# Kernel optimization log

Hardware: AMD Instinct MI355X
Metric: run time of the kernel (lower is better)

The kernel has to match this reference:

```python
import jax, jax.numpy as jnp
import numpy as np

B, T, C, H, K = 4, 2048, 2048, 32, 64
CHUNK = 64  # matches `splits = 64` in the torch source
EPS = 0.00064


def setup_inputs() -> dict:
    key = jax.random.key(0)
    ks = jax.random.split(key, 16)
    return {
        "x": jax.random.normal(ks[0], (B, T, C), jnp.float32),
        "state": jax.random.normal(ks[1], (1, 1, C), jnp.float32) * 0.1,
        "wkvstate": jax.random.normal(ks[2], (H, K, K), jnp.float32) * 0.02,
        "time_mix_k": jax.random.uniform(ks[3], (1, 1, C), jnp.float32),
        "time_mix_v": jax.random.uniform(ks[4], (1, 1, C), jnp.float32),
        "time_mix_r": jax.random.uniform(ks[5], (1, 1, C), jnp.float32),
        "time_mix_g": jax.random.uniform(ks[6], (1, 1, C), jnp.float32),
        "time_decay": jax.random.normal(ks[7], (H, K), jnp.float32) * 0.5,
        "time_faaaa": jax.random.normal(ks[8], (H, K), jnp.float32) * 0.1,
        "w_r": jax.random.normal(ks[9], (C, C), jnp.float32) * 0.02,
        "w_k": jax.random.normal(ks[10], (C, C), jnp.float32) * 0.02,
        "w_v": jax.random.normal(ks[11], (C, C), jnp.float32) * 0.02,
        "w_g": jax.random.normal(ks[12], (C, C), jnp.float32) * 0.02,
        "w_o": jax.random.normal(ks[13], (C, C), jnp.float32) * 0.02,
        "ln_w": jnp.ones((C,), jnp.float32),
        "ln_b": jnp.zeros((C,), jnp.float32),
    }


def reference(x, state, wkvstate, time_mix_k, time_mix_v, time_mix_r, time_mix_g,
              time_decay, time_faaaa, w_r, w_k, w_v, w_g, w_o, ln_w, ln_b):
    Bx, Tx, Cx = x.shape
    Hx, Kx = time_decay.shape

    # TimeShift (training path): prepend learned state, drop last token
    xx = jnp.concatenate([jnp.broadcast_to(state, (Bx, 1, Cx)), x[:, :-1]], axis=1)
    xk = x * time_mix_k + xx * (1.0 - time_mix_k)
    xv = x * time_mix_v + xx * (1.0 - time_mix_v)
    xr = x * time_mix_r + xx * (1.0 - time_mix_r)
    xg = x * time_mix_g + xx * (1.0 - time_mix_g)

    g = jax.nn.silu(xg @ w_g.T)  # (B,T,C)

    def to_heads(t):  # (B,T,C) -> (B,H,T,K)
        return t.reshape(Bx, Tx, Hx, Kx).transpose(0, 2, 1, 3)

    r = to_heads(xr @ w_r.T)
    k = to_heads(xk @ w_k.T)
    v = to_heads(xv @ w_v.T)

    w = jnp.exp(-jnp.exp(time_decay))  # (H,K), per-channel decay in (0,1)
    t_idx = jnp.arange(Tx)
    wfor = w[None, :, None, :] ** t_idx[None, None, :, None]          # w^t
    wback = w[None, :, None, :] ** (Tx - 1 - t_idx)[None, None, :, None]  # w^(T-1-t)

    # contribution of the incoming wkv state: (r * w^t) @ S0
    base = jnp.einsum('bhtk,hkj->bhtj', r * wfor, wkvstate)
    # bonus (u) diagonal term: sum_k(k_t * u * r_t) * v_t
    base = base + jnp.sum(k * r * time_faaaa[None, :, None, :], axis=-1, keepdims=True) * v

    kw = k * wback  # k_t scaled by w^(T-1-t), as in the source

    # strict-past causal product on shifted slices (r[:,1:] vs kw/v[:,:-1]),
    # computed chunk-by-chunk exactly like the blocked tril loop.
    rr, kk, vv = r[:, :, 1:], kw[:, :, :-1], v[:, :, :-1]
    Tm = Tx - 1
    pad = (-Tm) % CHUNK
    pd = lambda a: jnp.pad(a, ((0, 0), (0, 0), (0, pad), (0, 0)))
    rr, kk, vv = pd(rr), pd(kk), pd(vv)
    nC = (Tm + pad) // CHUNK
    resh = lambda a: a.reshape(Bx, Hx, nC, CHUNK, Kx).transpose(2, 0, 1, 3, 4)
    rc_, kc_, vc_ = resh(rr), resh(kk), resh(vv)
    mask = jnp.tril(jnp.ones((CHUNK, CHUNK), bool))  # q <= p (inclusive) == tril(i-j) globally

    def step(S, inp):
        rc, kc, vc = inp  # (B,H,CHUNK,K)
        att = jnp.einsum('bhpk,bhqk->bhpq', rc, kc)
        att = jnp.where(mask, att, 0.0)
        out = jnp.einsum('bhpq,bhqk->bhpk', att, vc) + jnp.einsum('bhpk,bhkj->bhpj', rc, S)
        S = S + jnp.einsum('bhqk,bhqj->bhkj', kc, vc)
        return S, out

    S0 = jnp.zeros((Bx, Hx, Kx, Kx), x.dtype)
    _, outs = jax.lax.scan(step, S0, (rc_, kc_, vc_))  # (nC,B,H,CHUNK,K)
    intra = outs.transpose(1, 2, 0, 3, 4).reshape(Bx, Hx, nC * CHUNK, Kx)[:, :, :Tm]
    wkv = base.at[:, :, 1:].add(intra)  # (B,H,T,K)

    # GroupNorm(n_head groups) after a bf16 round-trip, as in the source
    y = wkv.transpose(0, 2, 1, 3)  # (B,T,H,K)
    y = y.astype(jnp.bfloat16).astype(jnp.float32)
    mu = jnp.mean(y, axis=-1, keepdims=True)
    var = jnp.var(y, axis=-1, keepdims=True)
    y = (y - mu) / jnp.sqrt(var + EPS)
    y = y * ln_w.reshape(Hx, Kx) + ln_b.reshape(Hx, Kx)
    y = y.reshape(Bx, Tx, Cx)

    return (y * g) @ w_o.T
```

## Files before the change

### kernel.cpp

```cpp
#include <hip/hip_runtime.h>

#define Bn 4
#define Tn 2048
#define Cn 2048
#define Hn 32
#define Mn 8192
#define EPSV 0.00064f
#define SEGS 16
#define ZTHR 96.f

typedef __attribute__((ext_vector_type(4))) float f32x4;
typedef _Float16 half4 __attribute__((ext_vector_type(4)));
typedef _Float16 half8 __attribute__((ext_vector_type(8)));

#if defined(__has_builtin)
#if __has_builtin(__builtin_amdgcn_fdot2)
#define HAS_FDOT2 1
#endif
#endif
#ifndef HAS_FDOT2
#define HAS_FDOT2 0
#endif

#define SWZ(row, col) ((col) ^ ((((row) >> 2) & 7) << 3))

__device__ __forceinline__ unsigned short f2bf(float f) {
  unsigned int u = __float_as_uint(f);
  u += 0x7fffu + ((u >> 16) & 1u);
  return (unsigned short)(u >> 16);
}
__device__ __forceinline__ float bf2f(unsigned short h) {
  return __uint_as_float(((unsigned int)h) << 16);
}

__device__ __forceinline__ float dot8(half8 a, half8 b, float acc) {
#if HAS_FDOT2
  acc = __builtin_amdgcn_fdot2(__builtin_shufflevector(a, a, 0, 1),
                               __builtin_shufflevector(b, b, 0, 1), acc, false);
  acc = __builtin_amdgcn_fdot2(__builtin_shufflevector(a, a, 2, 3),
                               __builtin_shufflevector(b, b, 2, 3), acc, false);
  acc = __builtin_amdgcn_fdot2(__builtin_shufflevector(a, a, 4, 5),
                               __builtin_shufflevector(b, b, 4, 5), acc, false);
  acc = __builtin_amdgcn_fdot2(__builtin_shufflevector(a, a, 6, 7),
                               __builtin_shufflevector(b, b, 6, 7), acc, false);
#else
#pragma unroll
  for (int i = 0; i < 8; ++i) acc += (float)a[i] * (float)b[i];
#endif
  return acc;
}

__global__ __launch_bounds__(256) void wcast_f16_kernel(
    const float* __restrict__ src, _Float16* __restrict__ dst) {
  const size_t e = ((size_t)blockIdx.x * 256 + threadIdx.x) * 4;
  const float4 v = *(const float4*)(src + e);
  half4 h;
  h.x = (_Float16)v.x; h.y = (_Float16)v.y; h.z = (_Float16)v.z; h.w = (_Float16)v.w;
  *(half4*)(dst + e) = h;
}

__global__ __launch_bounds__(256) void mix4_kernel(
    const float* __restrict__ x, const float* __restrict__ state,
    const float* __restrict__ tmr, const float* __restrict__ tmk,
    const float* __restrict__ tmv, const float* __restrict__ tmg,
    _Float16* __restrict__ xr, _Float16* __restrict__ xk,
    _Float16* __restrict__ xv, _Float16* __restrict__ xg) {
  const size_t e = ((size_t)blockIdx.x * 256 + threadIdx.x) * 4;
  const int c = (int)(e & (Cn - 1));
  const int t = (int)((e >> 11) & (Tn - 1));
  float4 xv_ = *(const float4*)(x + e);
  float4 xx  = (t == 0) ? *(const float4*)(state + c) : *(const float4*)(x + e - Cn);
  float4 dx; dx.x = xv_.x - xx.x; dx.y = xv_.y - xx.y; dx.z = xv_.z - xx.z; dx.w = xv_.w - xx.w;
  const float* tms[4] = {tmr, tmk, tmv, tmg};
  _Float16* dsts[4] = {xr, xk, xv, xg};
#pragma unroll
  for (int s = 0; s < 4; ++s) {
    float4 m = *(const float4*)(tms[s] + c);
    half4 o;
    o.x = (_Float16)(xx.x + dx.x * m.x);
    o.y = (_Float16)(xx.y + dx.y * m.y);
    o.z = (_Float16)(xx.z + dx.z * m.z);
    o.w = (_Float16)(xx.w + dx.w * m.w);
    *(half4*)(dsts[s] + e) = o;
  }
}

template <int OUT_F16>
__global__ __launch_bounds__(512, 2) void gemm256_kernel(
    const _Float16* __restrict__ A, const _Float16* __restrict__ W,
    void* __restrict__ Ov) {
  __shared__ _Float16 As[4][256 * 32];
  __shared__ _Float16 Bs[4][256 * 32];
  const int tid = threadIdx.x;
  const int wid = tid >> 6, ln = tid & 63;
  const int wm = wid >> 2, wn = wid & 3;
  const int m16 = ln & 15, qd = ln >> 4;

  const int bid = blockIdx.x;
  const int mtile = ((bid & 7) << 2) | ((bid >> 3) & 3);
  const int ntile = bid >> 5;

  const _Float16* Ab = A + (size_t)mtile * 256 * Cn;
  const _Float16* Wb = W + (size_t)ntile * 256 * Cn;

  const _Float16* gA[2]; const _Float16* gB[2];
  int lof[2];
#pragma unroll
  for (int i = 0; i < 2; ++i) {
    int r = ((wid * 2 + i) << 4) + (ln >> 2);
    int q = (ln & 3) ^ ((ln >> 2) & 3) ^ ((ln >> 4) & 3);
    gA[i] = Ab + (size_t)r * Cn + (q << 3);
    gB[i] = Wb + (size_t)r * Cn + (q << 3);
    lof[i] = ((wid * 2 + i) << 10);
  }
  const int swz = (qd ^ (m16 & 3) ^ ((m16 >> 2) & 3)) << 4;
  const int aob = (wm * 128 + m16) * 64 + swz;
  const int bob = (wn * 64 + m16) * 64 + swz;

  f32x4 acc[8][4];
#pragma unroll
  for (int i = 0; i < 8; ++i)
#pragma unroll
    for (int j = 0; j < 4; ++j) acc[i][j] = 0.f;

#define STAGE(slot, k0)                                                              \
  {                                                                                  \
    _Pragma("unroll") for (int i_ = 0; i_ < 2; ++i_) {                               \
      __builtin_amdgcn_global_load_lds(                                              \
          (const __attribute__((address_space(1))) void*)(gA[i_] + (k0)),            \
          (__attribute__((address_space(3))) void*)((char*)&As[slot][0] + lof[i_]),  \
          16, 0, 0);                                                                 \
      __builtin_amdgcn_global_load_lds(                                              \
          (const __attribute__((address_space(1))) void*)(gB[i_] + (k0)),            \
          (__attribute__((address_space(3))) void*)((char*)&Bs[slot][0] + lof[i_]),  \
          16, 0, 0);                                                                 \
    }                                                                                \
  }

  STAGE(0, 0);
  STAGE(1, 32);

  const int NT = Cn / 32;
  for (int t = 0; t < NT; ++t) {
    const int sl = t & 3;
    if (t + 2 < NT) {
      STAGE((t + 2) & 3, (t + 2) * 32);
      asm volatile("s_waitcnt vmcnt(8)" ::: "memory");
    } else if (t + 1 < NT) {
      asm volatile("s_waitcnt vmcnt(4)" ::: "memory");
    } else {
      asm volatile("s_waitcnt vmcnt(0)" ::: "memory");
    }
    __builtin_amdgcn_s_barrier();

    const char* Abase = (const char*)&As[sl][0];
    const char* Bbase = (const char*)&Bs[sl][0];
    half8 bfr[4];
#pragma unroll
    for (int nf = 0; nf < 4; ++nf)
      bfr[nf] = *(const half8*)(Bbase + nf * 1024 + bob);
    half8 af[8];
#pragma unroll
    for (int fr = 0; fr < 8; ++fr)
      af[fr] = *(const half8*)(Abase + fr * 1024 + aob);
    __builtin_amdgcn_s_setprio(1);
#pragma unroll
    for (int fr = 0; fr < 8; ++fr)
#pragma unroll
      for (int nf = 0; nf < 4; ++nf)
        acc[fr][nf] = __builtin_amdgcn_mfma_f32_16x16x32_f16(af[fr], bfr[nf], acc[fr][nf], 0, 0, 0);
    __builtin_amdgcn_s_setprio(0);
  }
#undef STAGE

  const size_t obase = (size_t)mtile * 256 * Cn + (size_t)ntile * 256;
#pragma unroll
  for (int fr = 0; fr < 8; ++fr) {
#pragma unroll
    for (int nf = 0; nf < 4; ++nf) {
      int col  = wn * 64 + nf * 16 + m16;
      int row0 = wm * 128 + fr * 16 + (qd << 2);
      f32x4 cv = acc[fr][nf];
      if constexpr (OUT_F16) {
        _Float16* Ob = (_Float16*)Ov + obase;
#pragma unroll
        for (int rg = 0; rg < 4; ++rg)
          Ob[(size_t)(row0 + rg) * Cn + col] = (_Float16)cv[rg];
      } else {
        float* Ob = (float*)Ov + obase;
#pragma unroll
        for (int rg = 0; rg < 4; ++rg)
          Ob[(size_t)(row0 + rg) * Cn + col] = cv[rg];
      }
    }
  }
}

__global__ __launch_bounds__(256) void seg_sum_kernel(
    const _Float16* __restrict__ kA, const _Float16* __restrict__ vA,
    const float* __restrict__ td, _Float16* __restrict__ segsum) {
  __shared__ float sK[32][68];
  __shared__ float sV[32][68];
  __shared__ float sEw[64];
  __shared__ float sEwMin;
  const int tid = threadIdx.x;
  const int bh = blockIdx.x;
  const int seg = SEGS - 1 - blockIdx.y;
  const int b = bh >> 5, h = bh & 31;
  const size_t colbase = (size_t)b * Tn * Cn + h * 64;
  const _Float16* kG = kA + colbase;
  const _Float16* vG = vA + colbase;

  if (tid < 64) sEw[tid] = __expf(td[h * 64 + tid]);
  __syncthreads();
  if (tid == 0) {
    float mn = sEw[0];
    for (int i = 1; i < 64; ++i) mn = fminf(mn, sEw[i]);
    sEwMin = mn;
  }
  __syncthreads();

  const int uk0 = (tid >> 4) << 2;
  const int uj0 = (tid & 15) << 2;
  float su[16];
#pragma unroll
  for (int i = 0; i < 16; ++i) su[i] = 0.f;

  const int c0 = seg * (64 / SEGS), c1 = c0 + (64 / SEGS);
  for (int c = c0; c < c1; ++c) {
    const int tb = c << 5;
    if ((float)(Tn - 32 - tb) * sEwMin >= ZTHR) continue;
#pragma unroll
    for (int rep = 0; rep < 2; ++rep) {
      int f4 = tid + (rep << 8);
      int row = f4 >> 4;
      int col = (f4 & 15) << 2;
      int t = tb + row;
      size_t off = (size_t)t * Cn + col;
      half4 ku = *(const half4*)(kG + off);
      half4 vu = *(const half4*)(vG + off);
      float4 vf; vf.x = (float)vu.x; vf.y = (float)vu.y; vf.z = (float)vu.z; vf.w = (float)vu.w;
      *(float4*)&sV[row][col] = vf;
      float e = (float)(Tn - 1 - t);
      float4 kw;
      kw.x = (float)ku.x * __expf(-e * sEw[col + 0]);
      kw.y = (float)ku.y * __expf(-e * sEw[col + 1]);
      kw.z = (float)ku.z * __expf(-e * sEw[col + 2]);
      kw.w = (float)ku.w * __expf(-e * sEw[col + 3]);
      *(float4*)&sK[row][col] = kw;
    }
    __syncthreads();
    for (int q = 0; q < 32; ++q) {
      float4 kq = *(const float4*)&sK[q][uk0];
      float4 vq = *(const float4*)&sV[q][uj0];
      su[0]  += kq.x * vq.x; su[1]  += kq.x * vq.y; su[2]  += kq.x * vq.z; su[3]  += kq.x * vq.w;
      su[4]  += kq.y * vq.x; su[5]  += kq.y * vq.y; su[6]  += kq.y * vq.z; su[7]  += kq.y * vq.w;
      su[8]  += kq.z * vq.x; su[9]  += kq.z * vq.y; su[10] += kq.z * vq.z; su[11] += kq.z * vq.w;
      su[12] += kq.w * vq.x; su[13] += kq.w * vq.y; su[14] += kq.w * vq.z; su[15] += kq.w * vq.w;
    }
    __syncthreads();
  }
  _Float16* dst = segsum + ((size_t)bh * SEGS + seg) * 4096;
#pragma unroll
  for (int i = 0; i < 4; ++i) {
    half4 s;
    s.x = (_Float16)su[i * 4 + 0]; s.y = (_Float16)su[i * 4 + 1];
    s.z = (_Float16)su[i * 4 + 2]; s.w = (_Float16)su[i * 4 + 3];
    *(half4*)(dst + (uk0 + i) * 64 + uj0) = s;
  }
}

__global__ __launch_bounds__(256) void scan_kernel(
    const _Float16* __restrict__ rA, const _Float16* __restrict__ kA,
    const _Float16* __restrict__ vA, const _Float16* __restrict__ gA,
    const float* __restrict__ wkvst, const float* __restrict__ td,
    const float* __restrict__ faaaa, const float* __restrict__ lnw,
    const float* __restrict__ lnb, const _Float16* __restrict__ segsum,
    _Float16* __restrict__ A2) {
  __shared__ __align__(16) _Float16 sR[32][72];
  __shared__ __align__(16) _Float16 sK[32][72];
  __shared__ __align__(16) _Float16 sV[32][72];
  __shared__ __align__(16) _Float16 sRW[32][72];
  __shared__ __align__(16) _Float16 sS0[64][72];
  __shared__ float sS[64][68];
  __shared__ float sAtt[32][36];
  __shared__ float sEw[64];
  __shared__ float sU[64];
  __shared__ float sDotP[32][8];
  __shared__ float sRedM[32][8];
  __shared__ float sRedQ[32][8];
  __shared__ float sMV[32][2];
  __shared__ float sEwMin;
  const int tid = threadIdx.x;
  const int bh = blockIdx.x;
  const int seg = SEGS - 1 - blockIdx.y;
  const int b = bh >> 5, h = bh & 31;
  const size_t colbase = (size_t)b * Tn * Cn + h * 64;
  const _Float16* rG = rA + colbase;
  const _Float16* kG = kA + colbase;
  const _Float16* vG = vA + colbase;
  const _Float16* gG = gA + colbase;
  _Float16* outG = A2 + colbase;

  if (tid < 64) {
    sEw[tid] = __expf(td[h * 64 + tid]);
    sU[tid]  = faaaa[h * 64 + tid];
  }
  {
    float4 acc4[4];
#pragma unroll
    for (int j = 0; j < 4; ++j) { acc4[j].x = 0.f; acc4[j].y = 0.f; acc4[j].z = 0.f; acc4[j].w = 0.f; }
    for (int sp = 0; sp < seg; ++sp) {
      const _Float16* basep = segsum + ((size_t)bh * SEGS + sp) * 4096;
#pragma unroll
      for (int j = 0; j < 4; ++j) {
        int f4 = tid + j * 256;
        int row = f4 >> 4, c4 = (f4 & 15) << 2;
        half4 m = *(const half4*)(basep + row * 64 + c4);
        acc4[j].x += (float)m.x; acc4[j].y += (float)m.y;
        acc4[j].z += (float)m.z; acc4[j].w += (float)m.w;
      }
    }
#pragma unroll
    for (int j = 0; j < 4; ++j) {
      int f4 = tid + j * 256;
      int row = f4 >> 4, c4 = (f4 & 15) << 2;
      *(float4*)&sS[row][c4] = acc4[j];
    }
    int row = tid >> 2, c0 = (tid & 3) << 4;
    const float* sp = wkvst + (size_t)h * 4096 + row * 64 + c0;
    float4 f0 = *(const float4*)(sp);
    float4 f1 = *(const float4*)(sp + 4);
    float4 f2 = *(const float4*)(sp + 8);
    float4 f3 = *(const float4*)(sp + 12);
    half8 h0, h1;
    h0[0] = (_Float16)f0.x; h0[1] = (_Float16)f0.y; h0[2] = (_Float16)f0.z; h0[3] = (_Float16)f0.w;
    h0[4] = (_Float16)f1.x; h0[5] = (_Float16)f1.y; h0[6] = (_Float16)f1.z; h0[7] = (_Float16)f1.w;
    h1[0] = (_Float16)f2.x; h1[1] = (_Float16)f2.y; h1[2] = (_Float16)f2.z; h1[3] = (_Float16)f2.w;
    h1[4] = (_Float16)f3.x; h1[5] = (_Float16)f3.y; h1[6] = (_Float16)f3.z; h1[7] = (_Float16)f3.w;
    *(half8*)&sS0[row][SWZ(row, c0)] = h0;
    *(half8*)&sS0[row][SWZ(row, c0 + 8)] = h1;
  }
  __syncthreads();
  if (tid == 0) {
    float mn = sEw[0];
    for (int i = 1; i < 64; ++i) mn = fminf(mn, sEw[i]);
    sEwMin = mn;
  }
  __syncthreads();

  const int ap  = tid >> 3;
  const int aq0 = (tid & 7) << 2;
  const int oj0 = (tid & 7) << 3;
  const int uk0 = (tid >> 4) << 2;
  const int uj0 = (tid & 15) << 2;
  const int srow = tid >> 3;
  const int scol = (tid & 7) << 3;
  float lw[8], lb[8];
#pragma unroll
  for (int i = 0; i < 8; ++i) { lw[i] = lnw[h * 64 + oj0 + i]; lb[i] = lnb[h * 64 + oj0 + i]; }

  bool snz = (seg > 0) && ((float)(Tn - seg * (Tn / SEGS)) * sEwMin < ZTHR);

  const int c0 = seg * (64 / SEGS), c1 = c0 + (64 / SEGS);
  for (int c = c0; c < c1; ++c) {
    const int tb = c << 5;
    const bool skipc  = ((float)(Tn - 32 - tb) * sEwMin) >= ZTHR;
    const bool active = ((float)tb * sEwMin) < 88.f;
    {
      int t = tb + srow;
      size_t off = (size_t)t * Cn + scol;
      half8 ru = *(const half8*)(rG + off);
      half8 ku = *(const half8*)(kG + off);
      half8 vu = *(const half8*)(vG + off);
      *(half8*)&sV[srow][SWZ(srow, scol)] = vu;
      float dp = 0.f;
#pragma unroll
      for (int i = 0; i < 8; ++i) dp += (float)ku[i] * (float)ru[i] * sU[scol + i];
      sDotP[srow][tid & 7] = dp;
      if (!skipc) {
        *(half8*)&sR[srow][SWZ(srow, scol)] = ru;
        float e = (float)(Tn - 1 - t);
        half8 kwh;
#pragma unroll
        for (int i = 0; i < 8; ++i)
          kwh[i] = (_Float16)((float)ku[i] * __expf(-e * sEw[scol + i]));
        *(half8*)&sK[srow][SWZ(srow, scol)] = kwh;
      }
      if (active) {
        float tt = (float)t;
        half8 rwh;
#pragma unroll
        for (int i = 0; i < 8; ++i)
          rwh[i] = (_Float16)((float)ru[i] * __expf(-tt * sEw[scol + i]));
        *(half8*)&sRW[srow][SWZ(srow, scol)] = rwh;
      }
    }
    __syncthreads();
    if (!skipc) {
      float a4[4] = {0.f, 0.f, 0.f, 0.f};
      for (int k = 0; k < 64; k += 8) {
        half8 rv = *(const half8*)&sR[ap][SWZ(ap, k)];
#pragma unroll
        for (int qq = 0; qq < 4; ++qq) {
          int row = aq0 + qq;
          half8 kv = *(const half8*)&sK[row][SWZ(row, k)];
          a4[qq] = dot8(rv, kv, a4[qq]);
        }
      }
#pragma unroll
      for (int qq = 0; qq < 4; ++qq)
        sAtt[ap][aq0 + qq] = ((aq0 + qq) < ap) ? a4[qq] : 0.f;
      __syncthreads();
    }
    float y[8];
    {
      float o[8];
#pragma unroll
      for (int i = 0; i < 8; ++i) o[i] = 0.f;
      if (!skipc) {
        for (int q = 0; q < 32; ++q) {
          float aw = sAtt[ap][q];
          half8 vv = *(const half8*)&sV[q][SWZ(q, oj0)];
#pragma unroll
          for (int i = 0; i < 8; ++i) o[i] += aw * (float)vv[i];
        }
      }
      if (snz) {
        for (int k8 = 0; k8 < 64; k8 += 8) {
          half8 rv = *(const half8*)&sR[ap][SWZ(ap, k8)];
#pragma unroll
          for (int kk = 0; kk < 8; ++kk) {
            float rw = (float)rv[kk];
            const float* srow_ = &sS[k8 + kk][oj0];
            float4 s0 = *(const float4*)(srow_);
            float4 s1 = *(const float4*)(srow_ + 4);
            o[0] += rw * s0.x; o[1] += rw * s0.y; o[2] += rw * s0.z; o[3] += rw * s0.w;
            o[4] += rw * s1.x; o[5] += rw * s1.y; o[6] += rw * s1.z; o[7] += rw * s1.w;
          }
        }
      }
      if (active) {
        for (int k8 = 0; k8 < 64; k8 += 8) {
          half8 rv = *(const half8*)&sRW[ap][SWZ(ap, k8)];
#pragma unroll
          for (int kk = 0; kk < 8; ++kk) {
            float rw = (float)rv[kk];
            int k = k8 + kk;
            half8 s08 = *(const half8*)&sS0[k][SWZ(k, oj0)];
#pragma unroll
            for (int i = 0; i < 8; ++i) o[i] += rw * (float)s08[i];
          }
        }
      }
      float dot = 0.f;
#pragma unroll
      for (int s = 0; s < 8; ++s) dot += sDotP[ap][s];
      half8 vme = *(const half8*)&sV[ap][SWZ(ap, oj0)];
#pragma unroll
      for (int i = 0; i < 8; ++i) o[i] += dot * (float)vme[i];
      float sm = 0.f, sq = 0.f;
#pragma unroll
      for (int i = 0; i < 8; ++i) {
        y[i] = bf2f(f2bf(o[i]));
        sm += y[i]; sq += y[i] * y[i];
      }
      sRedM[ap][tid & 7] = sm; sRedQ[ap][tid & 7] = sq;
    }
    __syncthreads();
    if ((tid & 7) == 0) {
      float sm = 0.f, sq = 0.f;
#pragma unroll
      for (int i = 0; i < 8; ++i) { sm += sRedM[ap][i]; sq += sRedQ[ap][i]; }
      float mu = sm * (1.f / 64.f);
      float var = sq * (1.f / 64.f) - mu * mu;
      sMV[ap][0] = mu; sMV[ap][1] = rsqrtf(var + EPSV);
    }
    __syncthreads();
    {
      float mu = sMV[ap][0], rs = sMV[ap][1];
      int t = tb + ap;
      size_t off = (size_t)t * Cn + oj0;
      half8 g8 = *(const half8*)(gG + off);
      half8 o8;
#pragma unroll
      for (int i = 0; i < 8; ++i) {
        float gv = (float)g8[i];
        float yn = (y[i] - mu) * rs * lw[i] + lb[i];
        float gs = gv / (1.f + __expf(-gv));
        o8[i] = (_Float16)(yn * gs);
      }
      *(half8*)(outG + off) = o8;
    }
    if (!skipc) {
      float su[16];
#pragma unroll
      for (int i = 0; i < 4; ++i) {
        float4 s = *(const float4*)&sS[uk0 + i][uj0];
        su[i * 4 + 0] = s.x; su[i * 4 + 1] = s.y; su[i * 4 + 2] = s.z; su[i * 4 + 3] = s.w;
      }
      for (int q = 0; q < 32; ++q) {
        half4 kq4 = *(const half4*)&sK[q][SWZ(q, uk0)];
        half4 vq4 = *(const half4*)&sV[q][SWZ(q, uj0)];
        float kx = (float)kq4.x, ky = (float)kq4.y, kz = (float)kq4.z, kw_ = (float)kq4.w;
        float vx = (float)vq4.x, vy = (float)vq4.y, vz = (float)vq4.z, vw = (float)vq4.w;
        su[0]  += kx * vx; su[1]  += kx * vy; su[2]  += kx * vz; su[3]  += kx * vw;
        su[4]  += ky * vx; su[5]  += ky * vy; su[6]  += ky * vz; su[7]  += ky * vw;
        su[8]  += kz * vx; su[9]  += kz * vy; su[10] += kz * vz; su[11] += kz * vw;
        su[12] += kw_ * vx; su[13] += kw_ * vy; su[14] += kw_ * vz; su[15] += kw_ * vw;
      }
#pragma unroll
      for (int i = 0; i < 4; ++i) {
        float4 s; s.x = su[i * 4 + 0]; s.y = su[i * 4 + 1]; s.z = su[i * 4 + 2]; s.w = su[i * 4 + 3];
        *(float4*)&sS[uk0 + i][uj0] = s;
      }
      snz = true;
      __syncthreads();
    }
  }
}

extern "C" void kernel_launch(void* const* d_in, const int* in_sizes, int n_in,
                              void* d_out, int out_size, void* d_ws, size_t ws_size,
                              hipStream_t stream) {
  const float* x     = (const float*)d_in[0];
  const float* state = (const float*)d_in[1];
  const float* wkvst = (const float*)d_in[2];
  const float* tmk   = (const float*)d_in[3];
  const float* tmv   = (const float*)d_in[4];
  const float* tmr   = (const float*)d_in[5];
  const float* tmg   = (const float*)d_in[6];
  const float* td    = (const float*)d_in[7];
  const float* faaaa = (const float*)d_in[8];
  const float* w_r   = (const float*)d_in[9];
  const float* w_k   = (const float*)d_in[10];
  const float* w_v   = (const float*)d_in[11];
  const float* w_g   = (const float*)d_in[12];
  const float* w_o   = (const float*)d_in[13];
  const float* ln_w  = (const float*)d_in[14];
  const float* ln_b  = (const float*)d_in[15];
  float* out = (float*)d_out;
  char* ws = (char*)d_ws;

  const size_t SLOT = 33554432;
  _Float16* wh   = (_Float16*)(ws);
  _Float16* M0   = (_Float16*)(ws + 16777216);
  _Float16* M1   = (_Float16*)(ws + 16777216 + SLOT);
  _Float16* M2   = (_Float16*)(ws + 16777216 + 2 * SLOT);
  _Float16* M3   = (_Float16*)(ws + 16777216 + 3 * SLOT);
  _Float16* Rbuf = (_Float16*)(ws + 16777216 + 4 * SLOT);
  _Float16* segsum = (_Float16*)(ws + 184549376);

  mix4_kernel<<<dim3(16384), 256, 0, stream>>>(x, state, tmr, tmk, tmv, tmg, M0, M1, M2, M3);

  const float* wsrc[4] = {w_r, w_k, w_v, w_g};
  const _Float16* asrc[4] = {M0, M1, M2, M3};
  _Float16* pdst[4] = {Rbuf, M0, M1, M2};

  for (int s = 0; s < 4; ++s) {
    wcast_f16_kernel<<<dim3(4096), 256, 0, stream>>>(wsrc[s], wh);
    gemm256_kernel<1><<<dim3(256), 512, 0, stream>>>(asrc[s], wh, pdst[s]);
  }
  _Float16* R = Rbuf;
  _Float16* K = M0;
  _Float16* V = M1;
  _Float16* G = M2;
  _Float16* A2 = M3;

  seg_sum_kernel<<<dim3(128, SEGS), 256, 0, stream>>>(K, V, td, segsum);
  scan_kernel<<<dim3(128, SEGS), 256, 0, stream>>>(R, K, V, G, wkvst, td, faaaa,
                                                   ln_w, ln_b, segsum, A2);

  wcast_f16_kernel<<<dim3(4096), 256, 0, stream>>>(w_o, wh);
  gemm256_kernel<0><<<dim3(256), 512, 0, stream>>>(A2, wh, out);

  (void)in_sizes; (void)n_in; (void)out_size; (void)ws_size;
}
```

Before: 731.9 us.

## Deepen GEMM prefetch to three stages and split loads across MFMA halves

The fp16 MFMA GEMM main loop now keeps three K-tiles in flight instead of two, using the fourth LDS slot. Each iteration splits the next tile's global-to-LDS loads into two halves, issued around the two halves of the MFMA block, so memory traffic interleaves with compute. The goal is to hide more global load latency and spread issue pressure. The cost is an extra workgroup barrier per K-step and tighter dependence on the hand-written vmcnt accounting.

After: 845.8 us. 15.6% more time.

```diff
diff --git a/kernel.cpp b/kernel.cpp
--- a/kernel.cpp
+++ b/kernel.cpp
@@ -123,28 +123,28 @@
 #pragma unroll
     for (int j = 0; j < 4; ++j) acc[i][j] = 0.f;
 
-#define STAGE(slot, k0)                                                              \
+#define STAGE_I(slot, k0, i_)                                                        \
   {                                                                                  \
-    _Pragma("unroll") for (int i_ = 0; i_ < 2; ++i_) {                               \
-      __builtin_amdgcn_global_load_lds(                                              \
-          (const __attribute__((address_space(1))) void*)(gA[i_] + (k0)),            \
-          (__attribute__((address_space(3))) void*)((char*)&As[slot][0] + lof[i_]),  \
-          16, 0, 0);                                                                 \
-      __builtin_amdgcn_global_load_lds(                                              \
-          (const __attribute__((address_space(1))) void*)(gB[i_] + (k0)),            \
-          (__attribute__((address_space(3))) void*)((char*)&Bs[slot][0] + lof[i_]),  \
-          16, 0, 0);                                                                 \
-    }                                                                                \
-  }
-
-  STAGE(0, 0);
-  STAGE(1, 32);
+    __builtin_amdgcn_global_load_lds(                                                \
+        (const __attribute__((address_space(1))) void*)(gA[i_] + (k0)),              \
+        (__attribute__((address_space(3))) void*)((char*)&As[slot][0] + lof[i_]),    \
+        16, 0, 0);                                                                   \
+    __builtin_amdgcn_global_load_lds(                                                \
+        (const __attribute__((address_space(1))) void*)(gB[i_] + (k0)),              \
+        (__attribute__((address_space(3))) void*)((char*)&Bs[slot][0] + lof[i_]),    \
+        16, 0, 0);                                                                   \
+  }
+
+  STAGE_I(0, 0, 0); STAGE_I(0, 0, 1);
+  STAGE_I(1, 32, 0); STAGE_I(1, 32, 1);
+  STAGE_I(2, 64, 0); STAGE_I(2, 64, 1);
 
   const int NT = Cn / 32;
   for (int t = 0; t < NT; ++t) {
     const int sl = t & 3;
+    const int pf = (t + 3) & 3;
+    const int pk = (t + 3) * 32;
     if (t + 2 < NT) {
-      STAGE((t + 2) & 3, (t + 2) * 32);
       asm volatile("s_waitcnt vmcnt(8)" ::: "memory");
     } else if (t + 1 < NT) {
       asm volatile("s_waitcnt vmcnt(4)" ::: "memory");
@@ -152,6 +152,7 @@
       asm volatile("s_waitcnt vmcnt(0)" ::: "memory");
     }
     __builtin_amdgcn_s_barrier();
+    if (t + 3 < NT) STAGE_I(pf, pk, 0);
 
     const char* Abase = (const char*)&As[sl][0];
     const char* Bbase = (const char*)&Bs[sl][0];
@@ -159,19 +160,36 @@
 #pragma unroll
     for (int nf = 0; nf < 4; ++nf)
       bfr[nf] = *(const half8*)(Bbase + nf * 1024 + bob);
-    half8 af[8];
-#pragma unroll
-    for (int fr = 0; fr < 8; ++fr)
-      af[fr] = *(const half8*)(Abase + fr * 1024 + aob);
-    __builtin_amdgcn_s_setprio(1);
-#pragma unroll
-    for (int fr = 0; fr < 8; ++fr)
-#pragma unroll
-      for (int nf = 0; nf < 4; ++nf)
-        acc[fr][nf] = __builtin_amdgcn_mfma_f32_16x16x32_f16(af[fr], bfr[nf], acc[fr][nf], 0, 0, 0);
-    __builtin_amdgcn_s_setprio(0);
-  }
-#undef STAGE
+    {
+      half8 af[4];
+#pragma unroll
+      for (int fr = 0; fr < 4; ++fr)
+        af[fr] = *(const half8*)(Abase + fr * 1024 + aob);
+      __builtin_amdgcn_s_setprio(1);
+#pragma unroll
+      for (int fr = 0; fr < 4; ++fr)
+#pragma unroll
+        for (int nf = 0; nf < 4; ++nf)
+          acc[fr][nf] = __builtin_amdgcn_mfma_f32_16x16x32_f16(af[fr], bfr[nf], acc[fr][nf], 0, 0, 0);
+      __builtin_amdgcn_s_setprio(0);
+    }
+    __builtin_amdgcn_s_barrier();
+    if (t + 3 < NT) STAGE_I(pf, pk, 1);
+    {
+      half8 af[4];
+#pragma unroll
+      for (int fr = 0; fr < 4; ++fr)
+        af[fr] = *(const half8*)(Abase + (fr + 4) * 1024 + aob);
+      __builtin_amdgcn_s_setprio(1);
+#pragma unroll
+      for (int fr = 0; fr < 4; ++fr)
+#pragma unroll
+        for (int nf = 0; nf < 4; ++nf)
+          acc[fr + 4][nf] = __builtin_amdgcn_mfma_f32_16x16x32_f16(af[fr], bfr[nf], acc[fr + 4][nf], 0, 0, 0);
+      __builtin_amdgcn_s_setprio(0);
+    }
+  }
+#undef STAGE_I
 
   const size_t obase = (size_t)mtile * 256 * Cn + (size_t)ntile * 256;
 #pragma unroll
```
